# Kernel tuning notes

Hardware: AMD Instinct MI355X
Metric: run time of the kernel (lower is better)

Reference implementation:

```python
import jax, jax.numpy as jnp
import numpy as np

B, F, H, E = 16384, 128, 16, 32

def setup_inputs() -> dict:
    key = jax.random.key(0)
    k1, k2, k3 = jax.random.split(key, 3)
    x = jax.random.normal(k1, (B, F), dtype=jnp.float32)
    # per-feature Dense(1->H): weight is [F, H] (input dim 1), bias [F, H]
    W1 = jax.random.normal(k2, (F, H), dtype=jnp.float32) * 0.5
    b1 = jnp.zeros((F, H), dtype=jnp.float32)
    # per-feature Dense(H->E)
    W2 = jax.random.normal(k3, (F, H, E), dtype=jnp.float32) * (1.0 / np.sqrt(H))
    b2 = jnp.zeros((F, E), dtype=jnp.float32)
    return {"x": x, "W1": W1, "b1": b1, "W2": W2, "b2": b2}

def reference(x, W1, b1, W2, b2):
    # x: [B, F] -> per-feature scalar input to each tiny MLP
    # hidden: [B, F, H] = relu(x * W1 + b1), broadcasting feature weights
    h = jax.nn.relu(x[:, :, None] * W1[None, :, :] + b1[None, :, :])
    # output: [B, F, E] via batched (per-feature) GEMM
    out = jnp.einsum('bfh,fhe->bfe', h, W2) + b2[None, :, :]
    return out
```

## Files before the change

### kernel.cpp

```cpp
#include <hip/hip_runtime.h>

#define F_      128
#define H_      16
#define E_      32
#define BTILE   64
#define FTILE   8
#define NTHREADS (FTILE * 64)

__global__ __launch_bounds__(NTHREADS, 4)
void nfe_kernel(const float* __restrict__ x,
                const float* __restrict__ W1,
                const float* __restrict__ b1,
                const float* __restrict__ W2,
                const float* __restrict__ b2,
                float* __restrict__ out)
{
    __shared__ float4 lds4[BTILE * FTILE * 8];

    const int tid  = threadIdx.x;
    const int wave = tid >> 6;
    const int lane = tid & 63;
    const int fblk = blockIdx.x;
    const int bblk = blockIdx.y;

    const int f = __builtin_amdgcn_readfirstlane(fblk * FTILE + wave);
    const int b = bblk * BTILE + lane;

    const float* __restrict__ w1f = W1 + f * H_;
    const float* __restrict__ b1f = b1 + f * H_;
    const float* __restrict__ w2f = W2 + f * (H_ * E_);
    const float* __restrict__ b2f = b2 + f * E_;

    const float xv = x[b * F_ + f];

    float h[H_];
#pragma unroll
    for (int j = 0; j < H_; ++j) {
        float t = fmaf(xv, w1f[j], b1f[j]);
        h[j] = fmaxf(t, 0.0f);
    }

    float acc[E_];
#pragma unroll
    for (int e = 0; e < E_; ++e) acc[e] = b2f[e];
#pragma unroll
    for (int j = 0; j < H_; ++j) {
#pragma unroll
        for (int e = 0; e < E_; ++e)
            acc[e] = fmaf(h[j], w2f[j * E_ + e], acc[e]);
    }

#pragma unroll
    for (int e4 = 0; e4 < 8; ++e4) {
        int idx4 = lane * (FTILE * 8) + wave * 8 + (e4 ^ (lane & 7));
        lds4[idx4] = make_float4(acc[e4 * 4 + 0], acc[e4 * 4 + 1],
                                 acc[e4 * 4 + 2], acc[e4 * 4 + 3]);
    }
    __syncthreads();

    float4* __restrict__ out4 = (float4*)out;
    const int base4 = (bblk * BTILE * F_ + fblk * FTILE) * (E_ / 4);
#pragma unroll
    for (int it = 0; it < 8; ++it) {
        int i4     = it * NTHREADS + tid;
        int bb     = i4 >> 6;
        int within = i4 & 63;
        int ff     = within >> 3;
        int e4     = within & 7;
        float4 v = lds4[bb * (FTILE * 8) + ff * 8 + (e4 ^ (bb & 7))];
        out4[base4 + bb * (F_ * E_ / 4) + within] = v;
    }
}

extern "C" void kernel_launch(void* const* d_in, const int* in_sizes, int n_in,
                              void* d_out, int out_size, void* d_ws, size_t ws_size,
                              hipStream_t stream) {
    const float* x  = (const float*)d_in[0];
    const float* W1 = (const float*)d_in[1];
    const float* b1 = (const float*)d_in[2];
    const float* W2 = (const float*)d_in[3];
    const float* b2 = (const float*)d_in[4];
    float* out = (float*)d_out;

    const int B = in_sizes[0] / F_;
    dim3 grid(F_ / FTILE, B / BTILE);
    nfe_kernel<<<grid, NTHREADS, 0, stream>>>(x, W1, b1, W2, b2, out);
}
```

Before: 62.61 us.

## Keep per-feature weights in registers and loop waves over batch rows

Restructures the kernel so each lane owns one feature and a four-wide slice of the output, holding W1, b1 and W2 slices in registers, while each wave iterates over 64 batch rows. Output vec4s are written directly with nontemporal stores, removing the LDS transpose and barrier. The grid shrinks to far fewer blocks, trading occupancy and parallelism for weight reuse and simpler coalesced stores; the hidden activation is recomputed redundantly across the 8 lanes sharing a feature.

```diff
diff --git a/kernel.cpp b/kernel.cpp
--- a/kernel.cpp
+++ b/kernel.cpp
@@ -1,11 +1,14 @@
 #include <hip/hip_runtime.h>
 
-#define F_      128
-#define H_      16
-#define E_      32
-#define BTILE   64
-#define FTILE   8
-#define NTHREADS (FTILE * 64)
+#define F_   128
+#define H_   16
+#define E_   32
+#define FG   8
+#define BPW  64
+#define WAVES 4
+#define NTHREADS (WAVES * 64)
+
+typedef float v4f __attribute__((ext_vector_type(4)));
 
 __global__ __launch_bounds__(NTHREADS, 4)
 void nfe_kernel(const float* __restrict__ x,
@@ -15,60 +18,53 @@
                 const float* __restrict__ b2,
                 float* __restrict__ out)
 {
-    __shared__ float4 lds4[BTILE * FTILE * 8];
-
     const int tid  = threadIdx.x;
     const int wave = tid >> 6;
     const int lane = tid & 63;
-    const int fblk = blockIdx.x;
-    const int bblk = blockIdx.y;
 
-    const int f = __builtin_amdgcn_readfirstlane(fblk * FTILE + wave);
-    const int b = bblk * BTILE + lane;
+    const int f0 = blockIdx.x * FG;
+    const int b0 = (blockIdx.y * WAVES + wave) * BPW;
 
-    const float* __restrict__ w1f = W1 + f * H_;
-    const float* __restrict__ b1f = b1 + f * H_;
-    const float* __restrict__ w2f = W2 + f * (H_ * E_);
-    const float* __restrict__ b2f = b2 + f * E_;
+    const int f  = f0 + (lane >> 3);
+    const int e4 = lane & 7;
 
-    const float xv = x[b * F_ + f];
+    float w1v[H_], b1v[H_];
+    {
+        const v4f* p1 = (const v4f*)(W1 + f * H_);
+        const v4f* p2 = (const v4f*)(b1 + f * H_);
+#pragma unroll
+        for (int q = 0; q < 4; ++q) {
+            v4f a = p1[q], c = p2[q];
+            w1v[q*4+0]=a.x; w1v[q*4+1]=a.y; w1v[q*4+2]=a.z; w1v[q*4+3]=a.w;
+            b1v[q*4+0]=c.x; b1v[q*4+1]=c.y; b1v[q*4+2]=c.z; b1v[q*4+3]=c.w;
+        }
+    }
+    v4f w2v[H_];
+#pragma unroll
+    for (int j = 0; j < H_; ++j)
+        w2v[j] = *(const v4f*)(W2 + (f * H_ + j) * E_ + e4 * 4);
+    const v4f b2v = *(const v4f*)(b2 + f * E_ + e4 * 4);
 
-    float h[H_];
+    const float* xp = x + b0 * F_ + f;
+    v4f* op = (v4f*)out + (size_t)b0 * (F_ * E_ / 4)
+            + f0 * (E_ / 4) + lane;
+
+    float xv_next = *xp;
+#pragma unroll 2
+    for (int i = 0; i < BPW; ++i) {
+        const float xv = xv_next;
+        if (i + 1 < BPW) xv_next = xp[(i + 1) * F_];
+
+        v4f acc = b2v;
 #pragma unroll
-    for (int j = 0; j < H_; ++j) {
-        float t = fmaf(xv, w1f[j], b1f[j]);
-        h[j] = fmaxf(t, 0.0f);
-    }
-
-    float acc[E_];
-#pragma unroll
-    for (int e = 0; e < E_; ++e) acc[e] = b2f[e];
-#pragma unroll
-    for (int j = 0; j < H_; ++j) {
-#pragma unroll
-        for (int e = 0; e < E_; ++e)
-            acc[e] = fmaf(h[j], w2f[j * E_ + e], acc[e]);
-    }
-
-#pragma unroll
-    for (int e4 = 0; e4 < 8; ++e4) {
-        int idx4 = lane * (FTILE * 8) + wave * 8 + (e4 ^ (lane & 7));
-        lds4[idx4] = make_float4(acc[e4 * 4 + 0], acc[e4 * 4 + 1],
-                                 acc[e4 * 4 + 2], acc[e4 * 4 + 3]);
-    }
-    __syncthreads();
-
-    float4* __restrict__ out4 = (float4*)out;
-    const int base4 = (bblk * BTILE * F_ + fblk * FTILE) * (E_ / 4);
-#pragma unroll
-    for (int it = 0; it < 8; ++it) {
-        int i4     = it * NTHREADS + tid;
-        int bb     = i4 >> 6;
-        int within = i4 & 63;
-        int ff     = within >> 3;
-        int e4     = within & 7;
-        float4 v = lds4[bb * (FTILE * 8) + ff * 8 + (e4 ^ (bb & 7))];
-        out4[base4 + bb * (F_ * E_ / 4) + within] = v;
+        for (int j = 0; j < H_; ++j) {
+            const float hj = fmaxf(fmaf(xv, w1v[j], b1v[j]), 0.0f);
+            acc.x = fmaf(hj, w2v[j].x, acc.x);
+            acc.y = fmaf(hj, w2v[j].y, acc.y);
+            acc.z = fmaf(hj, w2v[j].z, acc.z);
+            acc.w = fmaf(hj, w2v[j].w, acc.w);
+        }
+        __builtin_nontemporal_store(acc, op + i * (F_ * E_ / 4));
     }
 }
 
@@ -83,6 +79,6 @@
     float* out = (float*)d_out;
 
     const int B = in_sizes[0] / F_;
-    dim3 grid(F_ / FTILE, B / BTILE);
+    dim3 grid(F_ / FG, B / (BPW * WAVES));
     nfe_kernel<<<grid, NTHREADS, 0, stream>>>(x, W1, b1, W2, b2, out);
 }
```

Result: faster. 56.74 us (-9.4%).
